# Kernel tuning notes

Measured on AMD Instinct MI355X. Metric: run time of the kernel, lower is better.

The kernel has to match this reference:

```python
import jax, jax.numpy as jnp
import numpy as np

E = 8            # num_experts
DIM = 2880       # model dim
HID = 2880       # expert hidden dim (mlp1 outputs 2*HID, interleaved glu/linear)
T = 16384        # total dispatched tokens, evenly split across experts
SWIGLU_LIMIT = 7.0
ALPHA = 1.702


def swiglu(x, alpha=ALPHA, limit=SWIGLU_LIMIT):
    # interleaved: even channels -> glu gate, odd channels -> linear
    x_glu = x[..., ::2]
    x_lin = x[..., 1::2]
    x_glu = jnp.minimum(x_glu, limit)
    x_lin = jnp.clip(x_lin, -limit, limit)
    return x_glu * jax.nn.sigmoid(alpha * x_glu) * (x_lin + 1.0)


def setup_inputs() -> dict:
    key = jax.random.key(0)
    k1, k2, k3, k4, k5 = jax.random.split(key, 5)
    scale = 0.02
    x = jax.random.normal(k1, (T, DIM), dtype=jnp.float32)
    num_tokens_per_expert = jnp.full((E,), T // E, dtype=jnp.int64)
    mlp1_weight = jax.random.normal(k2, (E, 2 * HID, DIM), dtype=jnp.float32) * scale
    mlp1_bias = jax.random.normal(k3, (E, 2 * HID), dtype=jnp.float32) * scale
    mlp2_weight = jax.random.normal(k4, (E, DIM, HID), dtype=jnp.float32) * scale
    mlp2_bias = jax.random.normal(k5, (E, DIM), dtype=jnp.float32) * scale
    return {
        "x": x,
        "num_tokens_per_expert": num_tokens_per_expert,
        "mlp1_weight": mlp1_weight,
        "mlp1_bias": mlp1_bias,
        "mlp2_weight": mlp2_weight,
        "mlp2_bias": mlp2_bias,
    }


def reference(x, num_tokens_per_expert, mlp1_weight, mlp1_bias, mlp2_weight, mlp2_bias):
    # Equal token counts per expert (as constructed): grouped GEMM == batched GEMM
    # over a reshaped [E, T/E, DIM] view. tp_degree == 1 so ScaleBiasForward is identity.
    tpe = T // E
    xg = x.reshape(E, tpe, DIM)                                  # [E, t, D]
    h = jnp.einsum("etd,ehd->eth", xg, mlp1_weight)              # [E, t, 2H]
    h = h + mlp1_bias[:, None, :]
    h = swiglu(h)                                                # [E, t, H]
    out = jnp.einsum("eth,edh->etd", h, mlp2_weight)             # [E, t, D]
    out = out + mlp2_bias[:, None, :]
    return out.reshape(T, DIM)
```

## Files before the change

kernel.cpp:

```cpp
#include <hip/hip_runtime.h>
#include <hip/hip_bf16.h>


#define TT   16384
#define DIM_ 2880
#define HID_ 2880
#define NE   8
#define TPE  2048
#define KDIM 2880
#define NT   45
#define NX   ((long)TT * DIM_)
#define N1   ((long)NE * 2 * HID_ * DIM_)
#define N2   ((long)NE * DIM_ * HID_)

typedef __attribute__((ext_vector_type(8))) short short8;
typedef __attribute__((ext_vector_type(4))) float f32x4;

__device__ __forceinline__ unsigned short f2bf(float f) {
  unsigned u = __builtin_bit_cast(unsigned, f);
  u += 0x7fffu + ((u >> 16) & 1u);
  return (unsigned short)(u >> 16);
}

__device__ __forceinline__ void cvt8(const float* __restrict__ s,
                                     unsigned short* __restrict__ d) {
  float4 a = *(const float4*)s;
  float4 b = *(const float4*)(s + 4);
  union { unsigned short u[8]; short8 v; } r;
  r.u[0] = f2bf(a.x); r.u[1] = f2bf(a.y); r.u[2] = f2bf(a.z); r.u[3] = f2bf(a.w);
  r.u[4] = f2bf(b.x); r.u[5] = f2bf(b.y); r.u[6] = f2bf(b.z); r.u[7] = f2bf(b.w);
  *(short8*)d = r.v;
}

__global__ void __launch_bounds__(256) cvt_all(const float* __restrict__ x,
                                               const float* __restrict__ w1,
                                               const float* __restrict__ w2,
                                               unsigned short* __restrict__ xb,
                                               unsigned short* __restrict__ w1b,
                                               unsigned short* __restrict__ w2b) {
  long i = ((long)blockIdx.x * 256 + threadIdx.x) * 8;
  if (i < NX)           cvt8(x  + i,        xb  + i);
  else if (i < NX + N1) cvt8(w1 + (i - NX), w1b + (i - NX));
  else                  cvt8(w2 + (i - NX - N1), w2b + (i - NX - N1));
}

#define GLDS(gsrc, ldst) \
  __builtin_amdgcn_global_load_lds( \
      (const __attribute__((address_space(1))) unsigned int*)(gsrc), \
      (__attribute__((address_space(3))) unsigned int*)(ldst), 16, 0, 0)

#define MFMA_(a, b, c) __builtin_amdgcn_mfma_f32_16x16x32_bf16(a, b, c, 0, 0, 0)

__global__ void __launch_bounds__(256, 2) gemm1_128(const unsigned short* __restrict__ A,
                                                    const unsigned short* __restrict__ B,
                                                    const float* __restrict__ bias,
                                                    unsigned short* __restrict__ ha) {
  __shared__ unsigned short As[2][128 * 64];
  __shared__ unsigned short Bs[2][128 * 64];

  const int tid  = threadIdx.x;
  const int lane = tid & 63;
  const int wid  = tid >> 6;
  const int wr   = wid >> 1;
  const int wc   = wid & 1;
  const int e    = blockIdx.z;
  const int bid  = blockIdx.x;

  const int c  = bid & 7;
  const int l  = bid >> 3;
  const int m0 = (c * 2 + (l & 1)) * 128;
  const int n0 = (l >> 1) * 128;

  const int srow = tid >> 3;
  const int scol = ((tid & 7) ^ (srow & 7)) << 3;
  const unsigned short* Aexp = A + ((size_t)e * TPE + m0 + srow) * KDIM + scol;
  const unsigned short* Bexp = B + ((size_t)e * 5760 + n0 + srow) * KDIM + scol;

  auto stage = [&](int buf, int kt) {
    const unsigned short* asrc = Aexp + (size_t)kt * 64;
#pragma unroll
    for (int j = 0; j < 4; ++j)
      GLDS(asrc + (size_t)(j * 32) * KDIM, &As[buf][j * 2048 + tid * 8]);
    const unsigned short* bsrc = Bexp + (size_t)kt * 64;
#pragma unroll
    for (int j = 0; j < 4; ++j)
      GLDS(bsrc + (size_t)(j * 32) * KDIM, &Bs[buf][j * 2048 + tid * 8]);
  };

  const int arow = (wr * 64 + (lane & 15)) * 128;
  const int brow = (wc * 64 + (lane & 15)) * 128;
  const int swzb = (lane & 7) << 4;
  const int kb   = ((lane >> 4) & 3) * 16;
  const int c0 = kb ^ swzb;
  const int c1 = (64 + kb) ^ swzb;

  f32x4 acc[4][4] = {};

  stage(0, 0);
  stage(1, 1);
  asm volatile("s_waitcnt vmcnt(8)" ::: "memory");
  __builtin_amdgcn_s_barrier();

  for (int t = 0; t < NT; ++t) {
    const int cur = t & 1;
    const char* aB = (const char*)(&As[cur][0]) + arow;
    const char* bB = (const char*)(&Bs[cur][0]) + brow;

    short8 a0[4], a1[4], b0[4], b1[4];
#pragma unroll
    for (int fm = 0; fm < 4; ++fm) {
      a0[fm] = *(const short8*)(aB + fm * 2048 + c0);
      a1[fm] = *(const short8*)(aB + fm * 2048 + c1);
    }
#pragma unroll
    for (int fn = 0; fn < 4; ++fn) {
      b0[fn] = *(const short8*)(bB + fn * 2048 + c0);
      b1[fn] = *(const short8*)(bB + fn * 2048 + c1);
    }

#pragma unroll
    for (int fn = 0; fn < 4; ++fn)
#pragma unroll
      for (int fm = 0; fm < 4; ++fm)
        acc[fm][fn] = MFMA_(a0[fm], b0[fn], acc[fm][fn]);

    asm volatile("s_waitcnt lgkmcnt(0)" ::: "memory");
    __builtin_amdgcn_s_barrier();

    const bool more = (t + 2 < NT);
    if (more) stage(cur, t + 2);

    __builtin_amdgcn_s_setprio(1);
#pragma unroll
    for (int fn = 0; fn < 4; ++fn)
#pragma unroll
      for (int fm = 0; fm < 4; ++fm)
        acc[fm][fn] = MFMA_(a1[fm], b1[fn], acc[fm][fn]);
    __builtin_amdgcn_s_setprio(0);

    if (more) asm volatile("s_waitcnt vmcnt(8)" ::: "memory");
    else      asm volatile("s_waitcnt vmcnt(0)" ::: "memory");
    __builtin_amdgcn_s_barrier();
  }

  const float* be = bias + (size_t)e * 5760;
  unsigned short* hae = ha + (size_t)e * TPE * HID_;
#pragma unroll
  for (int fm = 0; fm < 4; ++fm)
#pragma unroll
    for (int fn = 0; fn < 4; ++fn) {
      const int col = n0 + wc * 64 + fn * 16 + (lane & 15);
      const float bc = be[col];
#pragma unroll
      for (int j = 0; j < 4; ++j) {
        const int row = m0 + wr * 64 + fm * 16 + (lane >> 4) * 4 + j;
        float v = acc[fm][fn][j] + bc;
        float p = __shfl_xor(v, 1);
        if (!(lane & 1)) {
          float g  = fminf(v, 7.0f);
          float l2 = fminf(fmaxf(p, -7.0f), 7.0f);
          float act = g / (1.0f + __expf(-1.702f * g)) * (l2 + 1.0f);
          hae[(size_t)row * HID_ + (col >> 1)] = f2bf(act);
        }
      }
    }
}

__global__ void __launch_bounds__(512, 2) gemm2k(const unsigned short* __restrict__ A,
                                                 const unsigned short* __restrict__ B,
                                                 const float* __restrict__ bias,
                                                 float* __restrict__ Cout,
                                                 int M, int N) {
  __shared__ unsigned short As[2][256 * 64];
  __shared__ unsigned short Bs[2][320 * 64];

  const int tid  = threadIdx.x;
  const int lane = tid & 63;
  const int wid  = tid >> 6;
  const int wr   = wid >> 2;
  const int wc   = wid & 3;
  const int e    = blockIdx.z;

  const int ntn   = N / 320;
  const int per_e = ntn * (M / 256);
  const int bid   = blockIdx.x;
  const int swz   = (bid & 7) * (per_e >> 3) + (bid >> 3);
  const int m0    = (swz / ntn) * 256;
  const int n0    = (swz % ntn) * 320;

  const int srow = tid >> 3;
  const int scol = ((tid & 7) ^ (srow & 7)) << 3;
  const unsigned short* Aexp = A + ((size_t)e * M + m0 + srow) * KDIM + scol;
  const unsigned short* Bexp = B + ((size_t)e * N + n0 + srow) * KDIM + scol;

  auto stage = [&](int buf, int kt) {
    const unsigned short* asrc = Aexp + (size_t)kt * 64;
#pragma unroll
    for (int j = 0; j < 4; ++j)
      GLDS(asrc + (size_t)(j * 64) * KDIM, &As[buf][j * 4096 + tid * 8]);
    const unsigned short* bsrc = Bexp + (size_t)kt * 64;
#pragma unroll
    for (int j = 0; j < 5; ++j)
      GLDS(bsrc + (size_t)(j * 64) * KDIM, &Bs[buf][j * 4096 + tid * 8]);
  };

  const int arow = (wr * 128 + (lane & 15)) * 128;
  const int brow = (wc * 80  + (lane & 15)) * 128;
  const int swzb = (lane & 7) << 4;
  const int kb   = ((lane >> 4) & 3) * 16;
  const int c0 = kb ^ swzb;
  const int c1 = (64 + kb) ^ swzb;

  f32x4 acc[8][5] = {};

  stage(0, 0);
  stage(1, 1);
  asm volatile("s_waitcnt vmcnt(9)" ::: "memory");
  __builtin_amdgcn_s_barrier();

  for (int t = 0; t < NT; ++t) {
    const int cur = t & 1;
    const char* aB = (const char*)(&As[cur][0]) + arow;
    const char* bB = (const char*)(&Bs[cur][0]) + brow;

    short8 a0[8], a1[8], b0[5], b1[5];
#pragma unroll
    for (int fm = 0; fm < 8; ++fm) {
      a0[fm] = *(const short8*)(aB + fm * 2048 + c0);
      a1[fm] = *(const short8*)(aB + fm * 2048 + c1);
    }
#pragma unroll
    for (int fn = 0; fn < 5; ++fn) {
      b0[fn] = *(const short8*)(bB + fn * 2048 + c0);
      b1[fn] = *(const short8*)(bB + fn * 2048 + c1);
    }

#pragma unroll
    for (int fn = 0; fn < 5; ++fn)
#pragma unroll
      for (int fm = 0; fm < 8; ++fm)
        acc[fm][fn] = MFMA_(a0[fm], b0[fn], acc[fm][fn]);

    asm volatile("s_waitcnt lgkmcnt(0)" ::: "memory");
    __builtin_amdgcn_s_barrier();

    const bool more = (t + 2 < NT);
    if (more) stage(cur, t + 2);

    __builtin_amdgcn_s_setprio(1);
#pragma unroll
    for (int fn = 0; fn < 5; ++fn)
#pragma unroll
      for (int fm = 0; fm < 8; ++fm)
        acc[fm][fn] = MFMA_(a1[fm], b1[fn], acc[fm][fn]);
    __builtin_amdgcn_s_setprio(0);

    if (more) asm volatile("s_waitcnt vmcnt(9)" ::: "memory");
    else      asm volatile("s_waitcnt vmcnt(0)" ::: "memory");
    __builtin_amdgcn_s_barrier();
  }

  const float* be = bias + (size_t)e * N;
  float* out = Cout + (size_t)e * (size_t)M * N;
#pragma unroll
  for (int fm = 0; fm < 8; ++fm)
#pragma unroll
    for (int fn = 0; fn < 5; ++fn) {
      const int col = n0 + wc * 80 + fn * 16 + (lane & 15);
      const float bc = be[col];
#pragma unroll
      for (int j = 0; j < 4; ++j) {
        const int row = m0 + wr * 128 + fm * 16 + (lane >> 4) * 4 + j;
        out[(size_t)row * N + col] = acc[fm][fn][j] + bc;
      }
    }
}

extern "C" void kernel_launch(void* const* d_in, const int* in_sizes, int n_in,
                              void* d_out, int out_size, void* d_ws, size_t ws_size,
                              hipStream_t stream) {
  const float* x  = (const float*)d_in[0];
  const float* w1 = (const float*)d_in[2];
  const float* b1 = (const float*)d_in[3];
  const float* w2 = (const float*)d_in[4];
  const float* b2 = (const float*)d_in[5];

  unsigned short* xb  = (unsigned short*)d_ws;
  unsigned short* w1b = xb  + NX;
  unsigned short* w2b = w1b + N1;
  unsigned short* ha  = w2b + N2;

  const long ntot = NX + N1 + N2;
  cvt_all<<<(int)(ntot / 2048), 256, 0, stream>>>(x, w1, w2, xb, w1b, w2b);

  dim3 g1(720, 1, NE);
  gemm1_128<<<g1, 256, 0, stream>>>(xb, w1b, b1, ha);

  dim3 g2((DIM_ / 320) * (TPE / 256), 1, NE);
  gemm2k<<<g2, 512, 0, stream>>>(ha, w2b, b2, (float*)d_out, TPE, DIM_);
}
```

Measured before the change: 1.283 ms.

## Enlarge gemm1 tile to 256x256 with 512 threads and K-step 32

Rewrites the first GEMM kernel so each block computes a 256x256 output tile with 8 waves (each wave 128x64) instead of a 128x128 tile with 4 waves. The K step drops from 64 to 32, which keeps LDS per block about the same, and it adds a new XOR swizzle plus clamped B-row loads and masked epilogue stores because 5760 is not a multiple of 256. The larger tile raises arithmetic intensity and cuts global and L2 traffic per FLOP. The cost is twice as many loop iterations and barriers, higher register pressure from 32 accumulators per thread, and a partly wasted last column tile.

```diff
diff --git a/kernel.cpp b/kernel.cpp
--- a/kernel.cpp
+++ b/kernel.cpp
@@ -8,7 +8,10 @@
 #define NE   8
 #define TPE  2048
 #define KDIM 2880
+#define NTK  90
 #define NT   45
+#define NB1  5760
+#define NT1P 23
 #define NX   ((long)TT * DIM_)
 #define N1   ((long)NE * 2 * HID_ * DIM_)
 #define N2   ((long)NE * DIM_ * HID_)
@@ -51,112 +54,104 @@
 
 #define MFMA_(a, b, c) __builtin_amdgcn_mfma_f32_16x16x32_bf16(a, b, c, 0, 0, 0)
 
-__global__ void __launch_bounds__(256, 2) gemm1_128(const unsigned short* __restrict__ A,
+__global__ void __launch_bounds__(512, 2) gemm1_k32(const unsigned short* __restrict__ A,
                                                     const unsigned short* __restrict__ B,
                                                     const float* __restrict__ bias,
                                                     unsigned short* __restrict__ ha) {
-  __shared__ unsigned short As[2][128 * 64];
-  __shared__ unsigned short Bs[2][128 * 64];
+  __shared__ unsigned short As[2][256 * 32];
+  __shared__ unsigned short Bs[2][256 * 32];
 
   const int tid  = threadIdx.x;
   const int lane = tid & 63;
   const int wid  = tid >> 6;
-  const int wr   = wid >> 1;
-  const int wc   = wid & 1;
+  const int wr   = wid >> 2;
+  const int wc   = wid & 3;
   const int e    = blockIdx.z;
   const int bid  = blockIdx.x;
 
-  const int c  = bid & 7;
-  const int l  = bid >> 3;
-  const int m0 = (c * 2 + (l & 1)) * 128;
-  const int n0 = (l >> 1) * 128;
-
-  const int srow = tid >> 3;
-  const int scol = ((tid & 7) ^ (srow & 7)) << 3;
-  const unsigned short* Aexp = A + ((size_t)e * TPE + m0 + srow) * KDIM + scol;
-  const unsigned short* Bexp = B + ((size_t)e * 5760 + n0 + srow) * KDIM + scol;
+  const int m0 = (bid & 7) * 256;
+  const int n0 = (bid >> 3) * 256;
+
+  const int srow = (wid << 5) + (lane >> 2);
+  const int sc   = (((lane & 3) ^ ((lane >> 3) & 3)) << 3);
+  const unsigned short* Ae = A + ((size_t)e * TPE + m0 + srow) * KDIM + sc;
+  const unsigned short* Be = B + (size_t)e * NB1 * KDIM + sc;
+  const int brow0 = n0 + srow;
 
   auto stage = [&](int buf, int kt) {
-    const unsigned short* asrc = Aexp + (size_t)kt * 64;
-#pragma unroll
-    for (int j = 0; j < 4; ++j)
-      GLDS(asrc + (size_t)(j * 32) * KDIM, &As[buf][j * 2048 + tid * 8]);
-    const unsigned short* bsrc = Bexp + (size_t)kt * 64;
-#pragma unroll
-    for (int j = 0; j < 4; ++j)
-      GLDS(bsrc + (size_t)(j * 32) * KDIM, &Bs[buf][j * 2048 + tid * 8]);
+#pragma unroll
+    for (int u = 0; u < 2; ++u) {
+      GLDS(Ae + (size_t)(u * 16) * KDIM + kt * 32,
+           &As[buf][(wid * 2 + u) * 512 + lane * 8]);
+      int gr = brow0 + u * 16;
+      gr = gr < NB1 ? gr : NB1 - 1;
+      GLDS(Be + (size_t)gr * KDIM + kt * 32,
+           &Bs[buf][(wid * 2 + u) * 512 + lane * 8]);
+    }
   };
 
-  const int arow = (wr * 64 + (lane & 15)) * 128;
-  const int brow = (wc * 64 + (lane & 15)) * 128;
-  const int swzb = (lane & 7) << 4;
-  const int kb   = ((lane >> 4) & 3) * 16;
-  const int c0 = kb ^ swzb;
-  const int c1 = (64 + kb) ^ swzb;
-
-  f32x4 acc[4][4] = {};
+  const int kx   = (((lane >> 4) ^ ((lane >> 1) & 3)) << 4);
+  const int arow = (wr * 128 + (lane & 15)) * 64 + kx;
+  const int brow = (wc * 64  + (lane & 15)) * 64 + kx;
+
+  f32x4 acc[8][4] = {};
 
   stage(0, 0);
   stage(1, 1);
-  asm volatile("s_waitcnt vmcnt(8)" ::: "memory");
+  asm volatile("s_waitcnt vmcnt(4)" ::: "memory");
   __builtin_amdgcn_s_barrier();
 
-  for (int t = 0; t < NT; ++t) {
+  for (int t = 0; t < NTK; ++t) {
     const int cur = t & 1;
     const char* aB = (const char*)(&As[cur][0]) + arow;
     const char* bB = (const char*)(&Bs[cur][0]) + brow;
 
-    short8 a0[4], a1[4], b0[4], b1[4];
-#pragma unroll
-    for (int fm = 0; fm < 4; ++fm) {
-      a0[fm] = *(const short8*)(aB + fm * 2048 + c0);
-      a1[fm] = *(const short8*)(aB + fm * 2048 + c1);
-    }
-#pragma unroll
-    for (int fn = 0; fn < 4; ++fn) {
-      b0[fn] = *(const short8*)(bB + fn * 2048 + c0);
-      b1[fn] = *(const short8*)(bB + fn * 2048 + c1);
-    }
-
-#pragma unroll
-    for (int fn = 0; fn < 4; ++fn)
-#pragma unroll
-      for (int fm = 0; fm < 4; ++fm)
-        acc[fm][fn] = MFMA_(a0[fm], b0[fn], acc[fm][fn]);
+    short8 a[8], b[4];
+#pragma unroll
+    for (int fm = 0; fm < 8; ++fm) a[fm] = *(const short8*)(aB + fm * 1024);
+#pragma unroll
+    for (int fn = 0; fn < 4; ++fn) b[fn] = *(const short8*)(bB + fn * 1024);
+
+#pragma unroll
+    for (int fn = 0; fn < 2; ++fn)
+#pragma unroll
+      for (int fm = 0; fm < 8; ++fm)
+        acc[fm][fn] = MFMA_(a[fm], b[fn], acc[fm][fn]);
 
     asm volatile("s_waitcnt lgkmcnt(0)" ::: "memory");
     __builtin_amdgcn_s_barrier();
 
-    const bool more = (t + 2 < NT);
+    const bool more = (t + 2 < NTK);
     if (more) stage(cur, t + 2);
 
     __builtin_amdgcn_s_setprio(1);
 #pragma unroll
-    for (int fn = 0; fn < 4; ++fn)
-#pragma unroll
-      for (int fm = 0; fm < 4; ++fm)
-        acc[fm][fn] = MFMA_(a1[fm], b1[fn], acc[fm][fn]);
+    for (int fn = 2; fn < 4; ++fn)
+#pragma unroll
+      for (int fm = 0; fm < 8; ++fm)
+        acc[fm][fn] = MFMA_(a[fm], b[fn], acc[fm][fn]);
     __builtin_amdgcn_s_setprio(0);
 
-    if (more) asm volatile("s_waitcnt vmcnt(8)" ::: "memory");
+    if (more) asm volatile("s_waitcnt vmcnt(4)" ::: "memory");
     else      asm volatile("s_waitcnt vmcnt(0)" ::: "memory");
     __builtin_amdgcn_s_barrier();
   }
 
-  const float* be = bias + (size_t)e * 5760;
+  const float* be = bias + (size_t)e * NB1;
   unsigned short* hae = ha + (size_t)e * TPE * HID_;
 #pragma unroll
-  for (int fm = 0; fm < 4; ++fm)
+  for (int fm = 0; fm < 8; ++fm)
 #pragma unroll
     for (int fn = 0; fn < 4; ++fn) {
       const int col = n0 + wc * 64 + fn * 16 + (lane & 15);
-      const float bc = be[col];
+      const bool ok = col < NB1;
+      const float bc = ok ? be[col] : 0.0f;
 #pragma unroll
       for (int j = 0; j < 4; ++j) {
-        const int row = m0 + wr * 64 + fm * 16 + (lane >> 4) * 4 + j;
+        const int row = m0 + wr * 128 + fm * 16 + (lane >> 4) * 4 + j;
         float v = acc[fm][fn][j] + bc;
         float p = __shfl_xor(v, 1);
-        if (!(lane & 1)) {
+        if (!(lane & 1) && ok) {
           float g  = fminf(v, 7.0f);
           float l2 = fminf(fmaxf(p, -7.0f), 7.0f);
           float act = g / (1.0f + __expf(-1.702f * g)) * (l2 + 1.0f);
@@ -293,8 +288,8 @@
   const long ntot = NX + N1 + N2;
   cvt_all<<<(int)(ntot / 2048), 256, 0, stream>>>(x, w1, w2, xb, w1b, w2b);
 
-  dim3 g1(720, 1, NE);
-  gemm1_128<<<g1, 256, 0, stream>>>(xb, w1b, b1, ha);
+  dim3 g1(8 * NT1P, 1, NE);
+  gemm1_k32<<<g1, 512, 0, stream>>>(xb, w1b, b1, ha);
 
   dim3 g2((DIM_ / 320) * (TPE / 256), 1, NE);
   gemm2k<<<g2, 512, 0, stream>>>(ha, w2b, b2, (float*)d_out, TPE, DIM_);
```

Result: no change. 1.303 ms (+1.5%).
